# Kernel optimization log

Hardware: AMD Instinct MI355X
Metric: run time of the kernel (lower is better)

## Reference

```python
import jax, jax.numpy as jnp
import numpy as np

N, D_IN, D, C, TOPK = 8192, 1024, 512, 2, 6
SCALE = D ** -0.5
LN_EPS = 1e-5


def setup_inputs() -> dict:
    key = jax.random.key(0)
    ks = jax.random.split(key, 20)
    s = 0.02
    p = {
        'x': jax.random.normal(ks[0], (N, D_IN), jnp.float32),
        'fc1_w': jax.random.normal(ks[1], (D_IN, D)) * s,
        'fc1_b': jnp.zeros((D,)),
        'wh_w': jax.random.normal(ks[2], (D, D)) * s,
        'wh_b': jnp.zeros((D,)),
        'wt_w': jax.random.normal(ks[3], (D, D)) * s,
        'wt_b': jnp.zeros((D,)),
        'lin1_w': jax.random.normal(ks[4], (D, D)) * s,
        'lin1_b': jnp.zeros((D,)),
        'lin2_w': jax.random.normal(ks[5], (D, D)) * s,
        'lin2_b': jnp.zeros((D,)),
        'att1_w': jax.random.normal(ks[6], (D, D // 2)) * s,
        'att1_b': jnp.zeros((D // 2,)),
        'att2_w': jax.random.normal(ks[7], (D // 2, 1)) * s,
        'att2_b': jnp.zeros((1,)),
        'ln_g': jnp.ones((D,)),
        'ln_b': jnp.zeros((D,)),
        'fc_w': jax.random.normal(ks[8], (D, C)) * s,
        'fc_b': jnp.zeros((C,)),
    }
    return p


def reference(x, fc1_w, fc1_b, wh_w, wh_b, wt_w, wt_b, lin1_w, lin1_b,
              lin2_w, lin2_b, att1_w, att1_b, att2_w, att2_b, ln_g, ln_b,
              fc_w, fc_b):
    # _fc1: Linear + ReLU (dropout = eval identity)
    h = jax.nn.relu(x @ fc1_w + fc1_b)                      # [N, D]
    h = (h + h.mean(axis=0, keepdims=True)) * 0.5
    e_h = h @ wh_w + wh_b                                   # [N, D]
    e_t = h @ wt_w + wt_b                                   # [N, D]
    # dense N x N attention logits, then top-k neighbors
    logits = (e_h * SCALE) @ e_t.T                          # [N, N]
    tw, ti = jax.lax.top_k(logits, TOPK)                    # [N, K]
    Nb_h = e_t[ti]                                          # [N, K, D] gather
    p = jax.nn.softmax(tw, axis=-1)                         # [N, K]
    # eh_r = p * Nb_h + (1 - p) * e_h  (the matmul in torch is a broadcast)
    eh_r = p[..., None] * Nb_h + (1.0 - p)[..., None] * e_h[:, None, :]
    gate = jnp.tanh(e_h[:, None, :] + eh_r)                 # [N, K, D]
    ka = jnp.einsum('nkd,nkd->nk', Nb_h, gate)              # [N, K]
    kp = jax.nn.softmax(ka, axis=-1)                        # [N, K]
    e_Nh = jnp.einsum('nk,nkd->nd', kp, Nb_h)               # [N, D]
    sum_e = jax.nn.leaky_relu((e_h + e_Nh) @ lin1_w + lin1_b)
    bi_e = jax.nn.leaky_relu((e_h * e_Nh) @ lin2_w + lin2_b)
    emb = sum_e + bi_e                                      # [N, D]
    # GlobalAttention readout over all N nodes (batch=None -> one graph)
    att = jax.nn.leaky_relu(emb @ att1_w + att1_b) @ att2_w + att2_b  # [N,1]
    a = jax.nn.softmax(att, axis=0)                         # [N, 1]
    pooled = jnp.sum(a * emb, axis=0, keepdims=True)        # [1, D]
    # LayerNorm
    mu = pooled.mean(axis=-1, keepdims=True)
    var = pooled.var(axis=-1, keepdims=True)
    ln = (pooled - mu) * jax.lax.rsqrt(var + LN_EPS) * ln_g + ln_b
    out = ln @ fc_w + fc_b                                  # [1, C]
    Y_prob = jax.nn.softmax(out, axis=-1)
    Y_hat = jnp.argmax(out, axis=-1, keepdims=True)
    return out, Y_prob, Y_hat
```

## Files before the change

### kernel.cpp

```cpp
#include <hip/hip_runtime.h>
#include <hip/hip_bf16.h>
#include <cstdint>
#include <math.h>

typedef unsigned short u16;
typedef unsigned int u32;
typedef __bf16 bh;
typedef bh bh8 __attribute__((ext_vector_type(8)));
typedef float f32x4 __attribute__((ext_vector_type(4)));

#define SCALE_F 0.04419417382415922f

__device__ __forceinline__ float bf2f(u16 u) {
    union { float f; unsigned int i; } v; v.i = ((unsigned int)u) << 16; return v.f;
}
__device__ __forceinline__ u16 f2bf(float f) {
    __hip_bfloat16 h = __float2bfloat16(f);
    return __builtin_bit_cast(u16, h);
}
__device__ __forceinline__ bh8 ld8_f32(const float* p) {
    float4 f0 = *(const float4*)p;
    float4 f1 = *(const float4*)(p + 4);
    bh8 r;
    r[0] = (bh)f0.x; r[1] = (bh)f0.y; r[2] = (bh)f0.z; r[3] = (bh)f0.w;
    r[4] = (bh)f1.x; r[5] = (bh)f1.y; r[6] = (bh)f1.z; r[7] = (bh)f1.w;
    return r;
}

__device__ __forceinline__ u32 ordf(float f) {
    u32 u = __float_as_uint(f);
    return u ^ ((u32)((int)u >> 31) | 0x80000000u);
}
__device__ __forceinline__ float unordf(u32 s) {
    u32 u = (s & 0x80000000u) ? (s ^ 0x80000000u) : ~s;
    return __uint_as_float(u);
}
__device__ __forceinline__ u32 pack_vi(float v, int inv_idx) {
    return (ordf(v) & 0xFFFFFF00u) | (u32)inv_idx;
}
__device__ __forceinline__ float unpack_v(u32 p) {
    return unordf(p & 0xFFFFFF00u);
}

__device__ __forceinline__ void gl_lds16(const u16* g, u16* l) {
    __builtin_amdgcn_global_load_lds(
        (const __attribute__((address_space(1))) void*)g,
        (__attribute__((address_space(3))) void*)l, 16, 0, 0);
}

__global__ void transpose_cvt(const float* s0, u16* d0, const float* s1, u16* d1,
                              const float* s2, u16* d2, const float* s3, u16* d3,
                              const float* s4, u16* d4, const float* s5, u16* d5,
                              const float* xs, u16* xd) {
    int b = blockIdx.x;
    if (b >= 1664) {
        int t = threadIdx.y * 32 + threadIdx.x;
        size_t i = ((size_t)(b - 1664) * 256 + t) * 8;
        *(bh8*)(xd + i) = ld8_f32(xs + i);
        return;
    }
    __shared__ float tsh[32][33];
    const float* src; u16* dst; int R, C, tt;
    if      (b < 512)  { src = s0; dst = d0; R = 1024; C = 512; tt = b; }
    else if (b < 768)  { src = s1; dst = d1; R = 512;  C = 512; tt = b - 512; }
    else if (b < 1024) { src = s2; dst = d2; R = 512;  C = 512; tt = b - 768; }
    else if (b < 1280) { src = s3; dst = d3; R = 512;  C = 512; tt = b - 1024; }
    else if (b < 1536) { src = s4; dst = d4; R = 512;  C = 512; tt = b - 1280; }
    else               { src = s5; dst = d5; R = 512;  C = 256; tt = b - 1536; }
    int ntx = C >> 5;
    int bx = (tt % ntx) * 32, by = (tt / ntx) * 32;
    int x = threadIdx.x, y = threadIdx.y;
    for (int i = 0; i < 32; i += 8)
        tsh[y + i][x] = src[(size_t)(by + y + i) * C + bx + x];
    __syncthreads();
    for (int i = 0; i < 32; i += 8)
        dst[(size_t)(bx + y + i) * R + by + x] = f2bf(tsh[x][y + i]);
}

template<int KT, int NF>
__device__ __forceinline__ void kloop64(const u16* __restrict__ Ag, const u16* __restrict__ Bg,
                                        u16* Alds, u16* Blds, f32x4 (&acc)[2][NF]) {
    const int tid = threadIdx.x;
    const int wave = tid >> 6, lane = tid & 63;
    const int lr = lane & 15, quad = lane >> 4;
    const int wm = (wave & 1) * 32, wn = (wave >> 1) * (NF * 16);
    const int r = tid >> 2;
    const int g8 = (((tid & 3) ^ ((tid >> 3) & 3))) * 8;
    const int kbr8 = (quad ^ ((lr >> 1) & 3)) * 8;
    const u16* ga  = Ag + (size_t)r * KT + g8;
    const u16* gb0 = Bg + (size_t)r * KT + g8;
    const u16* gb1 = gb0 + (size_t)64 * KT;
    u16* la = Alds + wave * 512;
    u16* lb = Blds + wave * 512;
    #pragma unroll
    for (int k0 = 0; k0 < KT; k0 += 32) {
        __syncthreads();
        gl_lds16(ga + k0, la);
        gl_lds16(gb0 + k0, lb);
        if (NF == 4) gl_lds16(gb1 + k0, lb + 2048);
        __syncthreads();
        bh8 af[2], bf_[NF];
        #pragma unroll
        for (int i = 0; i < 2; i++)
            af[i] = *(const bh8*)&Alds[(wm + i * 16 + lr) * 32 + kbr8];
        #pragma unroll
        for (int i = 0; i < NF; i++)
            bf_[i] = *(const bh8*)&Blds[(wn + i * 16 + lr) * 32 + kbr8];
        #pragma unroll
        for (int mi = 0; mi < 2; mi++)
            #pragma unroll
            for (int ni = 0; ni < NF; ni++)
                acc[mi][ni] = __builtin_amdgcn_mfma_f32_16x16x32_bf16(
                    af[mi], bf_[ni], acc[mi][ni], 0, 0, 0);
    }
}

template<int ACT, int F32OUT>
__device__ __forceinline__ void epilogue64(f32x4 (&acc)[2][2], const float* bias,
                                           float* Cf, u16* Cb, int N, int m0, int n0) {
    const int tid = threadIdx.x;
    const int wave = tid >> 6, lane = tid & 63;
    const int lr = lane & 15, quad = lane >> 4;
    const int wm = (wave & 1) * 32, wn = (wave >> 1) * 32;
    #pragma unroll
    for (int ni = 0; ni < 2; ni++) {
        int col = n0 + wn + ni * 16 + lr;
        float bs = bias[col];
        #pragma unroll
        for (int mi = 0; mi < 2; mi++) {
            #pragma unroll
            for (int i = 0; i < 4; i++) {
                int row = m0 + wm + mi * 16 + quad * 4 + i;
                float v = acc[mi][ni][i] + bs;
                if (ACT == 1) v = fmaxf(v, 0.0f);
                if (ACT == 2) v = (v > 0.0f) ? v : 0.01f * v;
                size_t o = (size_t)row * N + col;
                if (F32OUT) Cf[o] = v;
                else        Cb[o] = f2bf(v);
            }
        }
    }
}

template<int ACT, int F32OUT, int KT>
__global__ __launch_bounds__(256) void gemm64(
    const u16* __restrict__ A, const u16* __restrict__ B, const float* __restrict__ bias,
    float* __restrict__ Cf, u16* __restrict__ Cb, int N)
{
    __shared__ __align__(16) u16 Alds[64 * 32];
    __shared__ __align__(16) u16 Blds[64 * 32];
    const int m0 = blockIdx.y * 64, n0 = blockIdx.x * 64;
    f32x4 acc[2][2] = {};
    kloop64<KT, 2>(A + (size_t)m0 * KT, B + (size_t)n0 * KT, Alds, Blds, acc);
    epilogue64<ACT, F32OUT>(acc, bias, Cf, Cb, N, m0, n0);
}

template<int KT>
__device__ __forceinline__ void kloop128p(const u16* __restrict__ Ag,
                                          const u16* __restrict__ Bg,
                                          u16* lds, f32x4 (&acc)[4][4]) {
    const int tid = threadIdx.x;
    const int wave = tid >> 6, lane = tid & 63;
    const int lr = lane & 15, quad = lane >> 4;
    const int wm = (wave & 1) * 64, wn = (wave >> 1) * 64;
    const int r = tid >> 2;
    const int g8 = (((tid & 3) ^ ((tid >> 3) & 3))) * 8;
    const int kbr8 = (quad ^ ((lr >> 1) & 3)) * 8;
    const u16* ga0 = Ag + (size_t)r * KT + g8;
    const u16* ga1 = ga0 + (size_t)64 * KT;
    const u16* gb0 = Bg + (size_t)r * KT + g8;
    const u16* gb1 = gb0 + (size_t)64 * KT;
    const int wofs = wave * 512;
    constexpr int NT = KT / 32;
    gl_lds16(ga0,      lds + wofs);
    gl_lds16(ga1,      lds + wofs + 2048);
    gl_lds16(gb0,      lds + 4096 + wofs);
    gl_lds16(gb1,      lds + 4096 + wofs + 2048);
    gl_lds16(ga0 + 32, lds + 8192 + wofs);
    gl_lds16(ga1 + 32, lds + 8192 + wofs + 2048);
    gl_lds16(gb0 + 32, lds + 8192 + 4096 + wofs);
    gl_lds16(gb1 + 32, lds + 8192 + 4096 + wofs + 2048);
    #pragma unroll
    for (int t = 0; t < NT; t++) {
        if (t + 1 < NT) asm volatile("s_waitcnt vmcnt(4)" ::: "memory");
        else            asm volatile("s_waitcnt vmcnt(0)" ::: "memory");
        __builtin_amdgcn_s_barrier();
        if (t + 2 < NT) {
            const int k2 = (t + 2) * 32;
            u16* b = lds + ((t + 2) % 3) * 8192;
            gl_lds16(ga0 + k2, b + wofs);
            gl_lds16(ga1 + k2, b + wofs + 2048);
            gl_lds16(gb0 + k2, b + 4096 + wofs);
            gl_lds16(gb1 + k2, b + 4096 + wofs + 2048);
        }
        const u16* Ab = lds + (t % 3) * 8192;
        const u16* Bb = Ab + 4096;
        bh8 af[4], bf_[4];
        #pragma unroll
        for (int i = 0; i < 4; i++) {
            af[i]  = *(const bh8*)&Ab[(wm + i * 16 + lr) * 32 + kbr8];
            bf_[i] = *(const bh8*)&Bb[(wn + i * 16 + lr) * 32 + kbr8];
        }
        __builtin_amdgcn_s_setprio(1);
        #pragma unroll
        for (int mi = 0; mi < 4; mi++)
            #pragma unroll
            for (int ni = 0; ni < 4; ni++)
                acc[mi][ni] = __builtin_amdgcn_mfma_f32_16x16x32_bf16(
                    af[mi], bf_[ni], acc[mi][ni], 0, 0, 0);
        __builtin_amdgcn_s_setprio(0);
    }
}

template<int ACT, int F32OUT>
__device__ __forceinline__ void epilogue128(f32x4 (&acc)[4][4], const float* bias,
                                            float* Cf, u16* Cb, int N, int m0, int n0) {
    const int tid = threadIdx.x;
    const int wave = tid >> 6, lane = tid & 63;
    const int lr = lane & 15, quad = lane >> 4;
    const int wm = (wave & 1) * 64, wn = (wave >> 1) * 64;
    #pragma unroll
    for (int ni = 0; ni < 4; ni++) {
        int col = n0 + wn + ni * 16 + lr;
        float bs = bias[col];
        #pragma unroll
        for (int mi = 0; mi < 4; mi++) {
            #pragma unroll
            for (int i = 0; i < 4; i++) {
                int row = m0 + wm + mi * 16 + quad * 4 + i;
                float v = acc[mi][ni][i] + bs;
                if (ACT == 1) v = fmaxf(v, 0.0f);
                if (ACT == 2) v = (v > 0.0f) ? v : 0.01f * v;
                size_t o = (size_t)row * N + col;
                if (F32OUT) Cf[o] = v;
                else        Cb[o] = f2bf(v);
            }
        }
    }
}

template<int ACT, int F32OUT, int KT>
__global__ __launch_bounds__(256) void gemm128(
    const u16* __restrict__ A, const u16* __restrict__ B, const float* __restrict__ bias,
    float* __restrict__ Cf, u16* __restrict__ Cb, int N)
{
    __shared__ __align__(16) u16 ldsbuf[3 * 8192];
    const int m0 = blockIdx.y * 128, n0 = blockIdx.x * 128;
    f32x4 acc[4][4] = {};
    kloop128p<KT>(A + (size_t)m0 * KT, B + (size_t)n0 * KT, ldsbuf, acc);
    epilogue128<ACT, F32OUT>(acc, bias, Cf, Cb, N, m0, n0);
}

__global__ __launch_bounds__(256) void ehet128(
    const u16* __restrict__ A, const u16* __restrict__ Bh, const u16* __restrict__ Bt,
    const float* __restrict__ bh_, const float* __restrict__ bt_,
    u16* __restrict__ Oh, u16* __restrict__ Ot)
{
    __shared__ __align__(16) u16 ldsbuf[3 * 8192];
    const int bx = blockIdx.x;
    const int m0 = blockIdx.y * 128, n0 = (bx & 3) * 128;
    const u16* B = (bx < 4) ? Bh : Bt;
    const float* bias = (bx < 4) ? bh_ : bt_;
    u16* O = (bx < 4) ? Oh : Ot;
    f32x4 acc[4][4] = {};
    kloop128p<512>(A + (size_t)m0 * 512, B + (size_t)n0 * 512, ldsbuf, acc);
    epilogue128<0, 0>(acc, bias, nullptr, O, 512, m0, n0);
}

__global__ __launch_bounds__(256) void lin12_64(
    const u16* __restrict__ A1, const u16* __restrict__ B1, const float* __restrict__ b1,
    const u16* __restrict__ A2, const u16* __restrict__ B2, const float* __restrict__ b2,
    u16* __restrict__ O)
{
    __shared__ __align__(16) u16 Alds[64 * 32];
    __shared__ __align__(16) u16 Blds[64 * 32];
    const int m0 = blockIdx.y * 64, n0 = blockIdx.x * 64;
    f32x4 acc1[2][2] = {}, acc2[2][2] = {};
    kloop64<512, 2>(A1 + (size_t)m0 * 512, B1 + (size_t)n0 * 512, Alds, Blds, acc1);
    kloop64<512, 2>(A2 + (size_t)m0 * 512, B2 + (size_t)n0 * 512, Alds, Blds, acc2);
    const int tid = threadIdx.x;
    const int wave = tid >> 6, lane = tid & 63;
    const int lr = lane & 15, quad = lane >> 4;
    const int wm = (wave & 1) * 32, wn = (wave >> 1) * 32;
    #pragma unroll
    for (int ni = 0; ni < 2; ni++) {
        int col = n0 + wn + ni * 16 + lr;
        float bs1 = b1[col], bs2 = b2[col];
        #pragma unroll
        for (int mi = 0; mi < 2; mi++) {
            #pragma unroll
            for (int i = 0; i < 4; i++) {
                int row = m0 + wm + mi * 16 + quad * 4 + i;
                float v1 = acc1[mi][ni][i] + bs1;
                v1 = (v1 > 0.0f) ? v1 : 0.01f * v1;
                float v2 = acc2[mi][ni][i] + bs2;
                v2 = (v2 > 0.0f) ? v2 : 0.01f * v2;
                O[(size_t)row * 512 + col] = f2bf(v1 + v2);
            }
        }
    }
}

__global__ __launch_bounds__(256) void logits_topk(
    const u16* __restrict__ Ah, const u16* __restrict__ Bt, u32* __restrict__ tvp)
{
    __shared__ __align__(16) u16 ldsbuf[3 * 8192];
    u32* S = (u32*)ldsbuf;
    const int tid = threadIdx.x;
    const int m0 = blockIdx.y * 128;
    const int cb0 = blockIdx.x * 256;
    const int lane = tid & 63, wave = tid >> 6;
    const int wm1 = wave & 1;
    const int wn = (wave >> 1) * 64;
    const int lr = lane & 15, quad = lane >> 4;
    const int srow = tid >> 2, scg = tid & 3;

    u32 v[2][6] = {{0,0,0,0,0,0},{0,0,0,0,0,0}};

    for (int nt = 0; nt < 2; nt++) {
        if (nt) __syncthreads();
        f32x4 acc[4][4] = {};
        kloop128p<512>(Ah + (size_t)m0 * 512,
                       Bt + (size_t)(cb0 + nt * 128) * 512, ldsbuf, acc);
        #pragma unroll
        for (int half = 0; half < 2; half++) {
            __syncthreads();
            if (wm1 == half) {
                #pragma unroll
                for (int mi = 0; mi < 4; mi++)
                    #pragma unroll
                    for (int ni = 0; ni < 4; ni++)
                        #pragma unroll
                        for (int i = 0; i < 4; i++) {
                            int colLocal = nt * 128 + wn + ni * 16 + lr;
                            S[(mi * 16 + quad * 4 + i) * 129 + wn + ni * 16 + lr]
                                = pack_vi(acc[mi][ni][i], 255 - colLocal);
                        }
            }
            __syncthreads();
            const u32* Sr = &S[srow * 129 + scg * 8];
            #pragma unroll
            for (int ch = 0; ch < 4; ch++) {
                #pragma unroll
                for (int c = 0; c < 8; c++) {
                    u32 x = Sr[ch * 32 + c];
                    v[half][5] = max(v[half][5], min(v[half][4], x));
                    v[half][4] = max(v[half][4], min(v[half][3], x));
                    v[half][3] = max(v[half][3], min(v[half][2], x));
                    v[half][2] = max(v[half][2], min(v[half][1], x));
                    v[half][1] = max(v[half][1], min(v[half][0], x));
                    v[half][0] = max(v[half][0], x);
                }
            }
        }
    }
    #pragma unroll
    for (int half = 0; half < 2; half++) {
        __syncthreads();
        {
            u32* dst = &S[srow * 129 + scg * 6];
            #pragma unroll
            for (int j = 0; j < 6; j++) dst[j] = v[half][j];
        }
        __syncthreads();
        if (tid < 64) {
            u32 m0v = 0, m1v = 0, m2v = 0, m3v = 0, m4v = 0, m5v = 0;
            const u32* Sr = &S[tid * 129];
            #pragma unroll
            for (int s = 0; s < 24; s++) {
                u32 x = Sr[s];
                m5v = max(m5v, min(m4v, x));
                m4v = max(m4v, min(m3v, x));
                m3v = max(m3v, min(m2v, x));
                m2v = max(m2v, min(m1v, x));
                m1v = max(m1v, min(m0v, x));
                m0v = max(m0v, x);
            }
            u32* dst = tvp + (size_t)(m0 + half * 64 + tid) * 192 + blockIdx.x * 6;
            dst[0] = m0v; dst[1] = m1v; dst[2] = m2v;
            dst[3] = m3v; dst[4] = m4v; dst[5] = m5v;
        }
    }
}

__global__ void topk_merge(const u32* __restrict__ tvp,
                           float* __restrict__ tv, int* __restrict__ ti)
{
    int r = blockIdx.x * 64 + threadIdx.x;
    u32 v[6]; int ix[6];
    #pragma unroll
    for (int j = 0; j < 6; j++) { v[j] = 0; ix[j] = 0; }
    const u32* pv = tvp + (size_t)r * 192;
    for (int b = 0; b < 32; b++) {
        #pragma unroll
        for (int j2 = 0; j2 < 6; j2++) {
            u32 p = pv[b * 6 + j2];
            if (p <= v[5]) break;
            v[5] = p; ix[5] = b * 256 + 255 - (int)(p & 255u);
            #pragma unroll
            for (int j = 5; j > 0; j--) {
                if (v[j] > v[j - 1]) {
                    u32 tf = v[j]; v[j] = v[j - 1]; v[j - 1] = tf;
                    int tx = ix[j]; ix[j] = ix[j - 1]; ix[j - 1] = tx;
                }
            }
        }
    }
    #pragma unroll
    for (int j = 0; j < 6; j++) {
        tv[(size_t)r * 6 + j] = unpack_v(v[j]) * SCALE_F;
        ti[(size_t)r * 6 + j] = ix[j];
    }
}

__global__ __launch_bounds__(256) void neighbor_kernel(
    const u16* __restrict__ eH, const u16* __restrict__ eT,
    const float* __restrict__ tv, const int* __restrict__ ti,
    u16* __restrict__ s1, u16* __restrict__ s2)
{
    const int tid = threadIdx.x, wave = tid >> 6, lane = tid & 63;
    const int n = blockIdx.x * 4 + wave;
    float tw[6]; int id[6];
    #pragma unroll
    for (int j = 0; j < 6; j++) {
        tw[j] = tv[n * 6 + j];
        int t = ti[n * 6 + j];
        id[j] = ((unsigned)t < 8192u) ? t : 0;
    }
    float mx = tw[0];
    #pragma unroll
    for (int j = 1; j < 6; j++) mx = fmaxf(mx, tw[j]);
    float p[6]; float ps = 0.f;
    #pragma unroll
    for (int j = 0; j < 6; j++) { p[j] = __expf(tw[j] - mx); ps += p[j]; }
    float inv = 1.0f / ps;
    #pragma unroll
    for (int j = 0; j < 6; j++) p[j] *= inv;

    const size_t base = (size_t)n * 512 + lane * 8;
    float eh[8];
    { bh8 v = *(const bh8*)(eH + base);
      #pragma unroll
      for (int c = 0; c < 8; c++) eh[c] = (float)v[c]; }
    float nb[6][8];
    #pragma unroll
    for (int j = 0; j < 6; j++) {
        bh8 v = *(const bh8*)(eT + (size_t)id[j] * 512 + lane * 8);
        #pragma unroll
        for (int c = 0; c < 8; c++) nb[j][c] = (float)v[c];
    }
    float ka[6];
    #pragma unroll
    for (int j = 0; j < 6; j++) {
        float s = 0.f;
        #pragma unroll
        for (int c = 0; c < 8; c++) {
            float e = p[j] * nb[j][c] + (1.f - p[j]) * eh[c];
            float x = eh[c] + e;
            x = fminf(fmaxf(x, -15.f), 15.f);
            float ex = __expf(2.f * x);
            float g = 1.f - 2.f / (ex + 1.f);
            s += nb[j][c] * g;
        }
        #pragma unroll
        for (int off = 32; off > 0; off >>= 1) s += __shfl_down(s, off);
        ka[j] = __shfl(s, 0);
    }
    float m2 = ka[0];
    #pragma unroll
    for (int j = 1; j < 6; j++) m2 = fmaxf(m2, ka[j]);
    float kp[6]; float ks = 0.f;
    #pragma unroll
    for (int j = 0; j < 6; j++) { kp[j] = __expf(ka[j] - m2); ks += kp[j]; }
    float inv2 = 1.0f / ks;
    #pragma unroll
    for (int j = 0; j < 6; j++) kp[j] *= inv2;
    bh8 o1, o2;
    #pragma unroll
    for (int c = 0; c < 8; c++) {
        float eN = 0.f;
        #pragma unroll
        for (int j = 0; j < 6; j++) eN += kp[j] * nb[j][c];
        o1[c] = (bh)(eh[c] + eN);
        o2[c] = (bh)(eh[c] * eN);
    }
    *(bh8*)(s1 + base) = o1;
    *(bh8*)(s2 + base) = o2;
}

__global__ void colsum_kernel(const u16* __restrict__ h, float* __restrict__ colsum) {
    int tid = threadIdx.x;
    int n0 = blockIdx.x * 32;
    float a0 = 0.f, a1 = 0.f;
    for (int k = 0; k < 32; k++) {
        size_t b = (size_t)(n0 + k) * 512;
        a0 += bf2f(h[b + tid]); a1 += bf2f(h[b + tid + 256]);
    }
    atomicAdd(&colsum[tid], a0);
    atomicAdd(&colsum[tid + 256], a1);
}

__global__ void meanmix_kernel(u16* __restrict__ h, const float* __restrict__ colsum) {
    size_t i = ((size_t)blockIdx.x * 256 + threadIdx.x) * 8;
    int col = (int)(i & 511);
    union { int4 v; u16 s[8]; } u;
    u.v = *(const int4*)&h[i];
    #pragma unroll
    for (int j = 0; j < 8; j++)
        u.s[j] = f2bf((bf2f(u.s[j]) + colsum[col + j] * (1.0f / 8192.0f)) * 0.5f);
    *(int4*)&h[i] = u.v;
}

__global__ __launch_bounds__(256) void att2_kernel(
    const float* __restrict__ a1, const float* __restrict__ w,
    const float* __restrict__ b, float* __restrict__ att)
{
    int row = blockIdx.x * 4 + (threadIdx.x >> 6);
    int lane = threadIdx.x & 63;
    const float* pr = a1 + (size_t)row * 256;
    float s = 0.f;
    #pragma unroll
    for (int k = 0; k < 4; k++) { int c = lane + k * 64; s += pr[c] * w[c]; }
    #pragma unroll
    for (int off = 32; off > 0; off >>= 1) s += __shfl_down(s, off);
    if (lane == 0) att[row] = s + b[0];
}

__global__ void att_max(const float* __restrict__ att, u32* __restrict__ scal_u) {
    int i = blockIdx.x * 256 + threadIdx.x;
    int lane = threadIdx.x & 63;
    u32 o = ordf(att[i]);
    #pragma unroll
    for (int off = 32; off > 0; off >>= 1) o = max(o, (u32)__shfl_down((int)o, off));
    if (lane == 0) atomicMax(&scal_u[0], o);
}
__global__ void att_sum(const float* __restrict__ att, float* __restrict__ scal) {
    int i = blockIdx.x * 256 + threadIdx.x;
    int lane = threadIdx.x & 63;
    float mx = unordf(((const u32*)scal)[0]);
    float e = __expf(att[i] - mx);
    #pragma unroll
    for (int off = 32; off > 0; off >>= 1) e += __shfl_down(e, off);
    if (lane == 0) atomicAdd(&scal[1], e);
}

__global__ void pooled_kernel(const u16* __restrict__ emb, const float* __restrict__ att,
                              const float* __restrict__ scal, float* __restrict__ pooled) {
    int tid = threadIdx.x;
    int n0 = blockIdx.x * 32;
    float mx = unordf(((const u32*)scal)[0]);
    float inv = 1.0f / scal[1];
    float a0 = 0.f, a1 = 0.f;
    for (int k = 0; k < 32; k++) {
        int n = n0 + k;
        float w = __expf(att[n] - mx) * inv;
        size_t b = (size_t)n * 512;
        a0 += w * bf2f(emb[b + tid]);
        a1 += w * bf2f(emb[b + tid + 256]);
    }
    atomicAdd(&pooled[tid], a0);
    atomicAdd(&pooled[tid + 256], a1);
}

__global__ void final_kernel(const float* __restrict__ pooled,
                             const float* __restrict__ g, const float* __restrict__ bln,
                             const float* __restrict__ fcw, const float* __restrict__ fcb,
                             float* __restrict__ out) {
    __shared__ float red[256];
    int tid = threadIdx.x;
    float x0 = pooled[tid], x1 = pooled[tid + 256];
    red[tid] = x0 + x1; __syncthreads();
    for (int s = 128; s > 0; s >>= 1) { if (tid < s) red[tid] += red[tid + s]; __syncthreads(); }
    float mu = red[0] * (1.0f / 512.0f); __syncthreads();
    float d0 = x0 - mu, d1 = x1 - mu;
    red[tid] = d0 * d0 + d1 * d1; __syncthreads();
    for (int s = 128; s > 0; s >>= 1) { if (tid < s) red[tid] += red[tid + s]; __syncthreads(); }
    float var = red[0] * (1.0f / 512.0f); __syncthreads();
    float rstd = rsqrtf(var + 1e-5f);
    float l0 = d0 * rstd * g[tid]       + bln[tid];
    float l1 = d1 * rstd * g[tid + 256] + bln[tid + 256];
    red[tid] = l0 * fcw[tid * 2] + l1 * fcw[(tid + 256) * 2]; __syncthreads();
    for (int s = 128; s > 0; s >>= 1) { if (tid < s) red[tid] += red[tid + s]; __syncthreads(); }
    float o0 = red[0] + fcb[0]; __syncthreads();
    red[tid] = l0 * fcw[tid * 2 + 1] + l1 * fcw[(tid + 256) * 2 + 1]; __syncthreads();
    for (int s = 128; s > 0; s >>= 1) { if (tid < s) red[tid] += red[tid + s]; __syncthreads(); }
    float o1 = red[0] + fcb[1];
    if (tid == 0) {
        float m = fmaxf(o0, o1);
        float e0 = expf(o0 - m), e1 = expf(o1 - m);
        float se = e0 + e1;
        out[0] = o0;
        out[1] = o1;
        out[2] = e0 / se;
        out[3] = e1 / se;
        out[4] = (o0 >= o1) ? 0.0f : 1.0f;
    }
}

extern "C" void kernel_launch(void* const* d_in, const int* in_sizes, int n_in,
                              void* d_out, int out_size, void* d_ws, size_t ws_size,
                              hipStream_t stream)
{
    const float* x      = (const float*)d_in[0];
    const float* fc1_w  = (const float*)d_in[1];
    const float* fc1_b  = (const float*)d_in[2];
    const float* wh_w   = (const float*)d_in[3];
    const float* wh_b   = (const float*)d_in[4];
    const float* wt_w   = (const float*)d_in[5];
    const float* wt_b   = (const float*)d_in[6];
    const float* lin1_w = (const float*)d_in[7];
    const float* lin1_b = (const float*)d_in[8];
    const float* lin2_w = (const float*)d_in[9];
    const float* lin2_b = (const float*)d_in[10];
    const float* att1_w = (const float*)d_in[11];
    const float* att1_b = (const float*)d_in[12];
    const float* att2_w = (const float*)d_in[13];
    const float* att2_b = (const float*)d_in[14];
    const float* ln_g   = (const float*)d_in[15];
    const float* ln_b   = (const float*)d_in[16];
    const float* fc_w   = (const float*)d_in[17];
    const float* fc_b   = (const float*)d_in[18];
    float* out = (float*)d_out;
    char* ws = (char*)d_ws;

    u16*   fc1T   = (u16*)(ws + 0);
    u16*   whT    = (u16*)(ws + 1048576);
    u16*   wtT    = (u16*)(ws + 1572864);
    u16*   l1T    = (u16*)(ws + 2097152);
    u16*   l2T    = (u16*)(ws + 2621440);
    u16*   a1T    = (u16*)(ws + 3145728);
    float* tv     = (float*)(ws + 3407872);
    int*   ti     = (int*)(ws + 3604480);
    float* att    = (float*)(ws + 3801088);
    float* colsum = (float*)(ws + 3833856);
    float* pooled = (float*)(ws + 3835904);
    float* scal   = (float*)(ws + 3837952);
    u32*   tvp    = (u32*)(ws + 4194304);
    u16*   hbf    = (u16*)(ws + 14680064);
    u16*   ehbf   = (u16*)(ws + 23068672);
    u16*   etbf   = (u16*)(ws + 31457280);
    u16*   s2bf   = (u16*)(ws + 39845888);
    u16*   xbf    = (u16*)(ws + 23068672);
    float* a1f    = (float*)(ws + 23068672);

    transpose_cvt<<<5760, dim3(32, 8), 0, stream>>>(
        fc1_w, fc1T, wh_w, whT, wt_w, wtT, lin1_w, l1T, lin2_w, l2T, att1_w, a1T, x, xbf);
    hipMemsetAsync(colsum, 0, 4160, stream);

    gemm128<1, 0, 1024><<<dim3(4, 64), 256, 0, stream>>>(xbf, fc1T, fc1_b, nullptr, hbf, 512);
    colsum_kernel<<<256, 256, 0, stream>>>(hbf, colsum);
    meanmix_kernel<<<2048, 256, 0, stream>>>(hbf, colsum);

    ehet128<<<dim3(8, 64), 256, 0, stream>>>(hbf, whT, wtT, wh_b, wt_b, ehbf, etbf);

    logits_topk<<<dim3(32, 64), 256, 0, stream>>>(ehbf, etbf, tvp);
    topk_merge<<<128, 64, 0, stream>>>(tvp, tv, ti);

    neighbor_kernel<<<2048, 256, 0, stream>>>(ehbf, etbf, tv, ti, hbf, s2bf);

    lin12_64<<<dim3(8, 128), 256, 0, stream>>>(hbf, l1T, lin1_b, s2bf, l2T, lin2_b, etbf);

    gemm64<2, 1, 512><<<dim3(4, 128), 256, 0, stream>>>(etbf, a1T, att1_b, a1f, nullptr, 256);
    att2_kernel<<<2048, 256, 0, stream>>>(a1f, att2_w, att2_b, att);
    att_max<<<32, 256, 0, stream>>>(att, (u32*)scal);
    att_sum<<<32, 256, 0, stream>>>(att, scal);
    pooled_kernel<<<256, 256, 0, stream>>>(etbf, att, scal, pooled);

    final_kernel<<<1, 256, 0, stream>>>(pooled, ln_g, ln_b, fc_w, fc_b, out);
}
```

Baseline: 379.0 us.

## Widen logits tile to 128x256 per pass and swizzle blocks across XCDs

The fused logits+top-k kernel now computes the full 128x256 logits tile in one triple-buffered k-loop, with each wave holding a 64x128 accumulator. Before, it ran two 128x128 passes that reloaded the same A rows, so this raises reuse per LDS load and removes a second pipeline prologue. It also adds an XCD-aware block-index remap to the GEMM kernels so that neighbouring tiles sharing operands land on the same XCD's L2. In exchange, register use (128 accumulator floats) and LDS use (about 72KB per block) go up, which may limit occupancy even with the launch bound of two blocks per CU.

```diff
diff --git a/kernel.cpp b/kernel.cpp
--- a/kernel.cpp
+++ b/kernel.cpp
@@ -46,6 +46,12 @@
     __builtin_amdgcn_global_load_lds(
         (const __attribute__((address_space(1))) void*)g,
         (__attribute__((address_space(3))) void*)l, 16, 0, 0);
+}
+
+__device__ __forceinline__ void xcd_swz(int bid, int& x, int& y) {
+    int xcd = bid & 7, idx = bid >> 3;
+    x = idx >> 3;
+    y = xcd * 8 + (idx & 7);
 }
 
 __global__ void transpose_cvt(const float* s0, u16* d0, const float* s1, u16* d1,
@@ -239,13 +245,15 @@
     }
 }
 
-template<int ACT, int F32OUT, int KT>
+template<int ACT, int F32OUT, int KT, int GNX>
 __global__ __launch_bounds__(256) void gemm128(
     const u16* __restrict__ A, const u16* __restrict__ B, const float* __restrict__ bias,
     float* __restrict__ Cf, u16* __restrict__ Cb, int N)
 {
     __shared__ __align__(16) u16 ldsbuf[3 * 8192];
-    const int m0 = blockIdx.y * 128, n0 = blockIdx.x * 128;
+    int bx, by;
+    xcd_swz(blockIdx.y * GNX + blockIdx.x, bx, by);
+    const int m0 = by * 128, n0 = bx * 128;
     f32x4 acc[4][4] = {};
     kloop128p<KT>(A + (size_t)m0 * KT, B + (size_t)n0 * KT, ldsbuf, acc);
     epilogue128<ACT, F32OUT>(acc, bias, Cf, Cb, N, m0, n0);
@@ -257,8 +265,9 @@
     u16* __restrict__ Oh, u16* __restrict__ Ot)
 {
     __shared__ __align__(16) u16 ldsbuf[3 * 8192];
-    const int bx = blockIdx.x;
-    const int m0 = blockIdx.y * 128, n0 = (bx & 3) * 128;
+    int bx, by;
+    xcd_swz(blockIdx.y * 8 + blockIdx.x, bx, by);
+    const int m0 = by * 128, n0 = (bx & 3) * 128;
     const u16* B = (bx < 4) ? Bh : Bt;
     const float* bias = (bx < 4) ? bh_ : bt_;
     u16* O = (bx < 4) ? Oh : Ot;
@@ -301,40 +310,102 @@
     }
 }
 
-__global__ __launch_bounds__(256) void logits_topk(
+template<int KT>
+__device__ __forceinline__ void kloop256w(const u16* __restrict__ Ag,
+                                          const u16* __restrict__ Bg,
+                                          u16* lds, f32x4 (&acc)[4][8]) {
+    const int tid = threadIdx.x;
+    const int wave = tid >> 6, lane = tid & 63;
+    const int lr = lane & 15, quad = lane >> 4;
+    const int wm = (wave & 1) * 64;
+    const int r = tid >> 2;
+    const int g8 = (((tid & 3) ^ ((tid >> 3) & 3))) * 8;
+    const int kbr8 = (quad ^ ((lr >> 1) & 3)) * 8;
+    const u16* ga0 = Ag + (size_t)r * KT + g8;
+    const u16* ga1 = ga0 + (size_t)64 * KT;
+    const u16* gb0 = Bg + (size_t)r * KT + g8;
+    const u16* gb1 = gb0 + (size_t)64 * KT;
+    const u16* gb2 = gb0 + (size_t)128 * KT;
+    const u16* gb3 = gb0 + (size_t)192 * KT;
+    const int wofs = wave * 512;
+    constexpr int NT = KT / 32;
+    constexpr int BUF = 12288;
+    auto stage = [&](int t, int koff) {
+        u16* b = lds + (t % 3) * BUF;
+        gl_lds16(ga0 + koff, b + wofs);
+        gl_lds16(ga1 + koff, b + wofs + 2048);
+        gl_lds16(gb0 + koff, b + 4096 + wofs);
+        gl_lds16(gb1 + koff, b + 4096 + wofs + 2048);
+        gl_lds16(gb2 + koff, b + 8192 + wofs);
+        gl_lds16(gb3 + koff, b + 8192 + wofs + 2048);
+    };
+    stage(0, 0);
+    stage(1, 32);
+    #pragma unroll
+    for (int t = 0; t < NT; t++) {
+        if (t + 1 < NT) asm volatile("s_waitcnt vmcnt(6)" ::: "memory");
+        else            asm volatile("s_waitcnt vmcnt(0)" ::: "memory");
+        __builtin_amdgcn_s_barrier();
+        if (t + 2 < NT) stage(t + 2, (t + 2) * 32);
+        const u16* Ab = lds + (t % 3) * BUF;
+        const u16* Bb = Ab + 4096 + (wave >> 1) * 4096;
+        bh8 af[4];
+        #pragma unroll
+        for (int i = 0; i < 4; i++)
+            af[i] = *(const bh8*)&Ab[(wm + i * 16 + lr) * 32 + kbr8];
+        __builtin_amdgcn_s_setprio(1);
+        #pragma unroll
+        for (int g = 0; g < 2; g++) {
+            bh8 bf_[4];
+            #pragma unroll
+            for (int j = 0; j < 4; j++)
+                bf_[j] = *(const bh8*)&Bb[((g * 4 + j) * 16 + lr) * 32 + kbr8];
+            #pragma unroll
+            for (int mi = 0; mi < 4; mi++)
+                #pragma unroll
+                for (int j = 0; j < 4; j++)
+                    acc[mi][g * 4 + j] = __builtin_amdgcn_mfma_f32_16x16x32_bf16(
+                        af[mi], bf_[j], acc[mi][g * 4 + j], 0, 0, 0);
+        }
+        __builtin_amdgcn_s_setprio(0);
+    }
+}
+
+__global__ __launch_bounds__(256, 2) void logits_topk(
     const u16* __restrict__ Ah, const u16* __restrict__ Bt, u32* __restrict__ tvp)
 {
-    __shared__ __align__(16) u16 ldsbuf[3 * 8192];
+    __shared__ __align__(16) u16 ldsbuf[3 * 12288];
     u32* S = (u32*)ldsbuf;
     const int tid = threadIdx.x;
-    const int m0 = blockIdx.y * 128;
-    const int cb0 = blockIdx.x * 256;
+    int bx, by;
+    xcd_swz(blockIdx.y * 32 + blockIdx.x, bx, by);
+    const int m0 = by * 128;
+    const int cb0 = bx * 256;
     const int lane = tid & 63, wave = tid >> 6;
-    const int wm1 = wave & 1;
-    const int wn = (wave >> 1) * 64;
+    const int wh = wave & 1;
+    const int wnh = wave >> 1;
     const int lr = lane & 15, quad = lane >> 4;
     const int srow = tid >> 2, scg = tid & 3;
 
+    f32x4 acc[4][8] = {};
+    kloop256w<512>(Ah + (size_t)m0 * 512, Bt + (size_t)cb0 * 512, ldsbuf, acc);
+
     u32 v[2][6] = {{0,0,0,0,0,0},{0,0,0,0,0,0}};
-
-    for (int nt = 0; nt < 2; nt++) {
-        if (nt) __syncthreads();
-        f32x4 acc[4][4] = {};
-        kloop128p<512>(Ah + (size_t)m0 * 512,
-                       Bt + (size_t)(cb0 + nt * 128) * 512, ldsbuf, acc);
-        #pragma unroll
-        for (int half = 0; half < 2; half++) {
+    #pragma unroll
+    for (int h = 0; h < 2; h++) {
+        #pragma unroll
+        for (int nh = 0; nh < 2; nh++) {
             __syncthreads();
-            if (wm1 == half) {
+            if (wh == h && wnh == nh) {
                 #pragma unroll
                 for (int mi = 0; mi < 4; mi++)
                     #pragma unroll
-                    for (int ni = 0; ni < 4; ni++)
+                    for (int f = 0; f < 8; f++)
                         #pragma unroll
                         for (int i = 0; i < 4; i++) {
-                            int colLocal = nt * 128 + wn + ni * 16 + lr;
-                            S[(mi * 16 + quad * 4 + i) * 129 + wn + ni * 16 + lr]
-                                = pack_vi(acc[mi][ni][i], 255 - colLocal);
+                            int colLocal = nh * 128 + f * 16 + lr;
+                            S[(mi * 16 + quad * 4 + i) * 129 + f * 16 + lr]
+                                = pack_vi(acc[mi][f][i], 255 - colLocal);
                         }
             }
             __syncthreads();
@@ -344,23 +415,23 @@
                 #pragma unroll
                 for (int c = 0; c < 8; c++) {
                     u32 x = Sr[ch * 32 + c];
-                    v[half][5] = max(v[half][5], min(v[half][4], x));
-                    v[half][4] = max(v[half][4], min(v[half][3], x));
-                    v[half][3] = max(v[half][3], min(v[half][2], x));
-                    v[half][2] = max(v[half][2], min(v[half][1], x));
-                    v[half][1] = max(v[half][1], min(v[half][0], x));
-                    v[half][0] = max(v[half][0], x);
+                    v[h][5] = max(v[h][5], min(v[h][4], x));
+                    v[h][4] = max(v[h][4], min(v[h][3], x));
+                    v[h][3] = max(v[h][3], min(v[h][2], x));
+                    v[h][2] = max(v[h][2], min(v[h][1], x));
+                    v[h][1] = max(v[h][1], min(v[h][0], x));
+                    v[h][0] = max(v[h][0], x);
                 }
             }
         }
     }
     #pragma unroll
-    for (int half = 0; half < 2; half++) {
+    for (int h = 0; h < 2; h++) {
         __syncthreads();
         {
             u32* dst = &S[srow * 129 + scg * 6];
             #pragma unroll
-            for (int j = 0; j < 6; j++) dst[j] = v[half][j];
+            for (int j = 0; j < 6; j++) dst[j] = v[h][j];
         }
         __syncthreads();
         if (tid < 64) {
@@ -376,7 +447,7 @@
                 m1v = max(m1v, min(m0v, x));
                 m0v = max(m0v, x);
             }
-            u32* dst = tvp + (size_t)(m0 + half * 64 + tid) * 192 + blockIdx.x * 6;
+            u32* dst = tvp + (size_t)(m0 + h * 64 + tid) * 192 + bx * 6;
             dst[0] = m0v; dst[1] = m1v; dst[2] = m2v;
             dst[3] = m3v; dst[4] = m4v; dst[5] = m5v;
         }
@@ -647,7 +718,7 @@
         fc1_w, fc1T, wh_w, whT, wt_w, wtT, lin1_w, l1T, lin2_w, l2T, att1_w, a1T, x, xbf);
     hipMemsetAsync(colsum, 0, 4160, stream);
 
-    gemm128<1, 0, 1024><<<dim3(4, 64), 256, 0, stream>>>(xbf, fc1T, fc1_b, nullptr, hbf, 512);
+    gemm128<1, 0, 1024, 4><<<dim3(4, 64), 256, 0, stream>>>(xbf, fc1T, fc1_b, nullptr, hbf, 512);
     colsum_kernel<<<256, 256, 0, stream>>>(hbf, colsum);
     meanmix_kernel<<<2048, 256, 0, stream>>>(hbf, colsum);
 
```

Measured after the change: 350.6 us. 1.08x faster.
